# Kernel optimization log

Measured on AMD Instinct MI355X. Metric: run time of the kernel, lower is better.

The kernel has to match this reference:

```python
import jax, jax.numpy as jnp
import numpy as np

N_GRAPHS = 64
NEG_SLOPE = 0.01  # default LeakyReLU slope
BN_EPS = 1e-5


def setup_inputs() -> dict:
    key = jax.random.key(0)
    ks = jax.random.split(key, 16)
    N, E, F_IN, H, H2, OUT, L = 50000, 800000, 64, 128, 64, 8, 3
    return {
        "x": jax.random.normal(ks[0], (N, F_IN), jnp.float32),
        "edge_index": jax.random.randint(ks[1], (2, E), 0, N, jnp.int32),
        "batch": jnp.sort(jax.random.randint(ks[2], (N,), 0, N_GRAPHS, jnp.int32)),
        "W_emb": jax.random.normal(ks[3], (F_IN, H), jnp.float32) * 0.05,
        "b_emb": jnp.zeros((H,), jnp.float32),
        "convW": jax.random.normal(ks[4], (L, H, H), jnp.float32) * 0.05,
        "convB": jnp.zeros((L, H), jnp.float32),
        "bn_gamma": jax.random.uniform(ks[5], (L, H), jnp.float32) + 0.5,
        "bn_beta": jax.random.normal(ks[6], (L, H), jnp.float32) * 0.1,
        "bn_mean": jax.random.normal(ks[7], (L, H), jnp.float32) * 0.1,
        "bn_var": jax.random.uniform(ks[8], (L, H), jnp.float32) + 0.5,
        "W1": jax.random.normal(ks[9], (H, H2), jnp.float32) * 0.05,
        "b1": jnp.zeros((H2,), jnp.float32),
        "W2": jax.random.normal(ks[10], (H2, OUT), jnp.float32) * 0.05,
        "b2": jnp.zeros((OUT,), jnp.float32),
    }


def reference(x, edge_index, batch, W_emb, b_emb, convW, convB,
              bn_gamma, bn_beta, bn_mean, bn_var, W1, b1, W2, b2):
    N = x.shape[0]
    # GCN normalization with self-loops (computed once; identical per layer)
    loop = jnp.arange(N, dtype=edge_index.dtype)
    s = jnp.concatenate([edge_index[0], loop])  # [E+N]
    d = jnp.concatenate([edge_index[1], loop])
    deg = jax.ops.segment_sum(jnp.ones(d.shape, x.dtype), d, num_segments=N)
    dinv = jax.lax.rsqrt(deg)  # deg >= 1 thanks to self-loops
    norm = dinv[s] * dinv[d]  # [E+N]

    h = x @ W_emb + b_emb  # node embedding, [N, H]
    L = convW.shape[0]
    for i in range(L):
        m = h @ convW[i]  # linear transform, [N, H]
        # gather-weight-scatter: sum_{(s->d)} norm * m[s]
        agg = jax.ops.segment_sum(m[s] * norm[:, None], d, num_segments=N) + convB[i]
        # BatchNorm (eval mode, running stats)
        hbn = (agg - bn_mean[i]) * jax.lax.rsqrt(bn_var[i] + BN_EPS) * bn_gamma[i] + bn_beta[i]
        h = jnp.where(hbn > 0, hbn, NEG_SLOPE * hbn)  # LeakyReLU
        # dropout is identity in eval mode

    g = jax.ops.segment_sum(h, batch, num_segments=N_GRAPHS)  # global_add_pool, [G, H]
    z = g @ W1 + b1
    z = jnp.where(z > 0, z, NEG_SLOPE * z)
    return z @ W2 + b2  # [G, OUT]
```

## Files before the change

kernel.cpp:

```cpp
#include <hip/hip_runtime.h>

#define NEG 0.01f
#define HF 128
#define BK 64
#define PB 512
#define SEG 40

typedef __attribute__((ext_vector_type(8))) short bf8;
typedef __attribute__((ext_vector_type(4))) float f4;
typedef __attribute__((ext_vector_type(2))) float f2;

__device__ __forceinline__ unsigned short f2bf(float v) {
    unsigned u = __float_as_uint(v);
    u = (u + 0x7fff + ((u >> 16) & 1)) >> 16;
    return (unsigned short)u;
}

__global__ __launch_bounds__(256) void k_mega1(
        const int* __restrict__ src, const int* __restrict__ dst, int E,
        int* __restrict__ cellcnt, int2* __restrict__ binbuf,
        const float* __restrict__ x, const float* __restrict__ W_emb,
        const float* __restrict__ b_emb, short* __restrict__ hbuf, int N,
        const float* __restrict__ convW, short* __restrict__ wt_c, int L,
        int NBIN, int EB) {
    __shared__ short wt[128 * 88];
    __shared__ int lcur[256];
    const int bid = blockIdx.x;
    const int tid = threadIdx.x;

    if (bid < PB) {
        lcur[tid] = 0;
        __syncthreads();
        const int per = (E + PB - 1) / PB;
        const int e0 = bid * per;
        const int e1 = (e0 + per < E) ? e0 + per : E;
        for (int e = e0 + tid; e < e1; e += 256) {
            const int d = dst[e];
            const int b = d >> 8;
            const int p = atomicAdd(&lcur[b], 1);
            if (p < SEG)
                binbuf[((size_t)b * PB + bid) * SEG + p] = make_int2(src[e], d);
        }
        __syncthreads();
        if (tid < NBIN) {
            int c = lcur[tid];
            cellcnt[(size_t)tid * PB + bid] = c < SEG ? c : SEG;
        }
        return;
    }
    if (bid < PB + EB) {
        for (int i = tid; i < 128 * 64; i += 256) {
            const int n = i >> 6, k = i & 63;
            wt[n * 88 + k] = (short)f2bf(W_emb[(size_t)k * HF + n]);
        }
        __syncthreads();
        const int wid = tid >> 6, lane = tid & 63;
        const int lr = lane & 15, lk = lane >> 4;
        const int m0 = (bid - PB) * 64 + wid * 16;
        if (m0 >= N) return;
        const int arow_i = m0 + lr < N ? m0 + lr : N - 1;
        bf8 a[2];
        const float* arow = x + (size_t)arow_i * 64 + lk * 8;
#pragma unroll
        for (int kk = 0; kk < 2; ++kk) {
            const float4 p = *reinterpret_cast<const float4*>(arow + kk * 32);
            const float4 q = *reinterpret_cast<const float4*>(arow + kk * 32 + 4);
            bf8 t;
            t[0] = (short)f2bf(p.x); t[1] = (short)f2bf(p.y);
            t[2] = (short)f2bf(p.z); t[3] = (short)f2bf(p.w);
            t[4] = (short)f2bf(q.x); t[5] = (short)f2bf(q.y);
            t[6] = (short)f2bf(q.z); t[7] = (short)f2bf(q.w);
            a[kk] = t;
        }
#pragma unroll
        for (int n = 0; n < 8; ++n) {
            f4 acc = {0.f, 0.f, 0.f, 0.f};
            const short* brow = wt + (n * 16 + lr) * 88 + lk * 8;
#pragma unroll
            for (int kk = 0; kk < 2; ++kk) {
                const bf8 b = *reinterpret_cast<const bf8*>(brow + kk * 32);
                acc = __builtin_amdgcn_mfma_f32_16x16x32_bf16(a[kk], b, acc, 0, 0, 0);
            }
            const int col = n * 16 + lr;
            const float bs = b_emb[col];
#pragma unroll
            for (int r = 0; r < 4; ++r)
                hbuf[(size_t)(m0 + lk * 4 + r) * HF + col] = (short)f2bf(acc[r] + bs);
        }
        return;
    }
    const int i = (bid - PB - EB) * 256 + tid;
    const int per = HF * HF;
    if (i < L * per) {
        const int l = i / per, r = i % per;
        const int n = r / HF, k = r % HF;
        wt_c[i] = (short)f2bf(convW[(size_t)l * per + (size_t)k * HF + n]);
    }
}

__global__ __launch_bounds__(256) void k_binfill(
        const int* __restrict__ cellcnt, const int2* __restrict__ binbuf,
        int* __restrict__ bkt, int* __restrict__ cnt,
        float* __restrict__ gbuf, int NBIN) {
    const int bid = blockIdx.x;
    const int tid = threadIdx.x;
    if (bid >= NBIN) {
        for (int i = tid; i < 64 * HF; i += 256) gbuf[i] = 0.0f;
        return;
    }
    __shared__ int lcnt[256];
    lcnt[tid] = 0;
    __syncthreads();
    for (int sg = tid; sg < PB; sg += 256) {
        const int c = cellcnt[(size_t)bid * PB + sg];
        const int2* segp = binbuf + ((size_t)bid * PB + sg) * SEG;
        for (int i = 0; i < c; ++i) {
            const int2 ed = segp[i];
            const int p = atomicAdd(&lcnt[ed.y & 255], 1);
            if (p < BK) bkt[(size_t)ed.y * BK + p] = ed.x;
        }
    }
    __syncthreads();
    cnt[(bid << 8) + tid] = lcnt[tid];
}

__global__ __launch_bounds__(256) void k_gemm_conv(
        const short* __restrict__ A,
        const short* __restrict__ Bt,
        const int* __restrict__ cnt,
        short* __restrict__ C,
        int N) {
    const int tid = threadIdx.x;
    const int wid = tid >> 6, lane = tid & 63;
    const int lr = lane & 15, lk = lane >> 4;
    const int m0 = blockIdx.x * 128 + wid * 32;
    if (m0 >= N) return;
    bf8 aA[4], aB[4];
    const short* arowA = A + (size_t)(m0 + lr) * HF + lk * 8;
    const short* arowB = arowA + 16 * HF;
#pragma unroll
    for (int kk = 0; kk < 4; ++kk) {
        aA[kk] = *reinterpret_cast<const bf8*>(arowA + kk * 32);
        aB[kk] = *reinterpret_cast<const bf8*>(arowB + kk * 32);
    }
    float dvA[4], dvB[4];
#pragma unroll
    for (int r = 0; r < 4; ++r) {
        int rowA = m0 + lk * 4 + r;       if (rowA >= N) rowA = N - 1;
        int rowB = m0 + 16 + lk * 4 + r;  if (rowB >= N) rowB = N - 1;
        dvA[r] = rsqrtf((float)cnt[rowA] + 1.0f);
        dvB[r] = rsqrtf((float)cnt[rowB] + 1.0f);
    }
#pragma unroll
    for (int n = 0; n < 8; ++n) {
        f4 accA = {0.f, 0.f, 0.f, 0.f};
        f4 accB = {0.f, 0.f, 0.f, 0.f};
        const short* brow = Bt + (size_t)(n * 16 + lr) * HF + lk * 8;
#pragma unroll
        for (int kk = 0; kk < 4; ++kk) {
            const bf8 b = *reinterpret_cast<const bf8*>(brow + kk * 32);
            accA = __builtin_amdgcn_mfma_f32_16x16x32_bf16(aA[kk], b, accA, 0, 0, 0);
            accB = __builtin_amdgcn_mfma_f32_16x16x32_bf16(aB[kk], b, accB, 0, 0, 0);
        }
        const int col = n * 16 + lr;
#pragma unroll
        for (int r = 0; r < 4; ++r) {
            C[(size_t)(m0 + lk * 4 + r) * HF + col]      = (short)f2bf(accA[r] * dvA[r]);
            C[(size_t)(m0 + 16 + lk * 4 + r) * HF + col] = (short)f2bf(accB[r] * dvB[r]);
        }
    }
}

__global__ __launch_bounds__(256) void k_gather(
        const int* __restrict__ bkt, const int* __restrict__ cnt,
        const short* __restrict__ ms,
        const float* __restrict__ convB,
        const float* __restrict__ bn_g, const float* __restrict__ bn_b,
        const float* __restrict__ bn_m, const float* __restrict__ bn_v,
        short* __restrict__ h, int N) {
    const int wid  = (blockIdx.x * 256 + threadIdx.x) >> 6;
    const int lane = threadIdx.x & 63;
    const int sub  = lane >> 4;
    const int lf   = lane & 15;
    if (wid >= N) return;
    const size_t b0 = (size_t)wid * BK;
    const int myslot = bkt[b0 + lane];
    int deg = cnt[wid];
    if (deg > BK) deg = BK;

    f2 acc[4];
#pragma unroll
    for (int j = 0; j < 4; ++j) acc[j] = (f2){0.f, 0.f};
    union U { bf8 v; unsigned u[4]; };

    U self;
    self.v = *reinterpret_cast<const bf8*>(ms + (size_t)wid * HF + lf * 8);

    const int iters = (deg + 3) >> 2;
    int slot = sub;
    bool v0 = slot < deg;
    U r0;
    { const int s = v0 ? __shfl(myslot, slot) : wid;
      r0.v = *reinterpret_cast<const bf8*>(ms + (size_t)s * HF + lf * 8); }
    bool v1 = slot + 4 < deg;
    U r1;
    { const int s = v1 ? __shfl(myslot, slot + 4) : wid;
      r1.v = *reinterpret_cast<const bf8*>(ms + (size_t)s * HF + lf * 8); }
    for (int t = 0; t < iters; ++t) {
        const int sl2 = slot + 8;
        const bool v2 = sl2 < deg;
        const int s2 = v2 ? __shfl(myslot, sl2) : wid;
        U r2;
        r2.v = *reinterpret_cast<const bf8*>(ms + (size_t)s2 * HF + lf * 8);
        if (v0) {
#pragma unroll
            for (int j = 0; j < 4; ++j) {
                f2 val;
                val.x = __uint_as_float(r0.u[j] << 16);
                val.y = __uint_as_float(r0.u[j] & 0xffff0000u);
                acc[j] += val;
            }
        }
        r0 = r1; v0 = v1; r1 = r2; v1 = v2; slot += 4;
    }
    if (sub == 0) {
#pragma unroll
        for (int j = 0; j < 4; ++j) {
            f2 val;
            val.x = __uint_as_float(self.u[j] << 16);
            val.y = __uint_as_float(self.u[j] & 0xffff0000u);
            acc[j] += val;
        }
    }
#pragma unroll
    for (int j = 0; j < 4; ++j) {
        acc[j].x += __shfl_xor(acc[j].x, 16);
        acc[j].y += __shfl_xor(acc[j].y, 16);
        acc[j].x += __shfl_xor(acc[j].x, 32);
        acc[j].y += __shfl_xor(acc[j].y, 32);
    }
    if (sub == 0) {
        const float dv = rsqrtf((float)deg + 1.0f);
        const int f0 = lf * 8;
        unsigned ou[4];
#pragma unroll
        for (int j = 0; j < 4; ++j) {
            const int fx = f0 + 2 * j, fy = fx + 1;
            const float sx = rsqrtf(bn_v[fx] + 1e-5f) * bn_g[fx];
            const float sy = rsqrtf(bn_v[fy] + 1e-5f) * bn_g[fy];
            float vx = (dv * acc[j].x + convB[fx] - bn_m[fx]) * sx + bn_b[fx];
            float vy = (dv * acc[j].y + convB[fy] - bn_m[fy]) * sy + bn_b[fy];
            vx = vx > 0.0f ? vx : NEG * vx;
            vy = vy > 0.0f ? vy : NEG * vy;
            ou[j] = (unsigned)f2bf(vx) | ((unsigned)f2bf(vy) << 16);
        }
        *reinterpret_cast<uint4*>(h + (size_t)wid * HF + f0) =
            *reinterpret_cast<uint4*>(ou);
    }
}

__global__ __launch_bounds__(256) void k_pool(
        const short* __restrict__ h, const int* __restrict__ batch,
        float* __restrict__ g, int N, int per) {
    const int gwid = (blockIdx.x * 256 + threadIdx.x) >> 6;
    const int lane = threadIdx.x & 63;
    const int n0 = gwid * per;
    if (n0 >= N) return;
    const int n1 = (n0 + per < N) ? n0 + per : N;
    const int fp = lane * 2;
    float ax = 0.f, ay = 0.f;
    int cur = batch[n0];
    for (int n = n0; n < n1; ++n) {
        const int b = batch[n];
        if (b != cur) {
            atomicAdd(&g[cur * HF + fp], ax);
            atomicAdd(&g[cur * HF + fp + 1], ay);
            ax = 0.f; ay = 0.f; cur = b;
        }
        const unsigned u = *reinterpret_cast<const unsigned*>(h + (size_t)n * HF + fp);
        ax += __uint_as_float(u << 16);
        ay += __uint_as_float(u & 0xffff0000u);
    }
    atomicAdd(&g[cur * HF + fp], ax);
    atomicAdd(&g[cur * HF + fp + 1], ay);
}

__global__ __launch_bounds__(128) void k_mlp(
        const float* __restrict__ g, const float* __restrict__ W1,
        const float* __restrict__ b1, const float* __restrict__ W2,
        const float* __restrict__ b2, float* __restrict__ out) {
    __shared__ float gr[128];
    __shared__ float z[64];
    const int gid = blockIdx.x, t = threadIdx.x;
    gr[t] = g[gid * HF + t];
    __syncthreads();
    if (t < 64) {
        float acc = b1[t];
#pragma unroll 8
        for (int k = 0; k < 128; ++k) acc += gr[k] * W1[k * 64 + t];
        z[t] = acc > 0.0f ? acc : NEG * acc;
    }
    __syncthreads();
    if (t < 8) {
        float acc = b2[t];
#pragma unroll 8
        for (int j = 0; j < 64; ++j) acc += z[j] * W2[j * 8 + t];
        out[gid * 8 + t] = acc;
    }
}

extern "C" void kernel_launch(void* const* d_in, const int* in_sizes, int n_in,
                              void* d_out, int out_size, void* d_ws, size_t ws_size,
                              hipStream_t stream) {
    const float* x       = (const float*)d_in[0];
    const int*   eidx    = (const int*)  d_in[1];
    const int*   batch   = (const int*)  d_in[2];
    const float* W_emb   = (const float*)d_in[3];
    const float* b_emb   = (const float*)d_in[4];
    const float* convW   = (const float*)d_in[5];
    const float* convB   = (const float*)d_in[6];
    const float* bn_g    = (const float*)d_in[7];
    const float* bn_b    = (const float*)d_in[8];
    const float* bn_m    = (const float*)d_in[9];
    const float* bn_v    = (const float*)d_in[10];
    const float* W1      = (const float*)d_in[11];
    const float* b1      = (const float*)d_in[12];
    const float* W2      = (const float*)d_in[13];
    const float* b2      = (const float*)d_in[14];

    const int F_IN = 64;
    const int N = in_sizes[0] / F_IN;
    const int E = in_sizes[1] / 2;
    const int L = in_sizes[5] / (HF * HF);
    const int G = 64;

    const int* esrc = eidx;
    const int* edst = eidx + E;

    const int NBIN  = (N + 255) >> 8;
    const int Npad2 = NBIN << 8;
    const int Npad  = ((N + 127) / 128) * 128;

    int* bkt      = (int*)d_ws;
    int* cnt      = bkt + (size_t)Npad2 * BK;
    int* cellcnt  = cnt + Npad2;
    int2* binbuf  = (int2*)(cellcnt + (size_t)NBIN * PB);
    short* hbuf   = (short*)(binbuf + (size_t)NBIN * PB * SEG);
    short* ms     = hbuf + (size_t)Npad * HF;
    short* wt_c   = ms + (size_t)Npad * HF;
    float* gbuf   = (float*)(wt_c + (size_t)L * HF * HF);

    const int EB = (N + 63) / 64;
    const int WB = (L * HF * HF + 255) / 256;
    k_mega1<<<PB + EB + WB, 256, 0, stream>>>(
        esrc, edst, E, cellcnt, binbuf, x, W_emb, b_emb, hbuf, N,
        convW, wt_c, L, NBIN, EB);

    k_binfill<<<NBIN + 1, 256, 0, stream>>>(cellcnt, binbuf, bkt, cnt, gbuf, NBIN);

    for (int i = 0; i < L; ++i) {
        k_gemm_conv<<<(N + 127) / 128, 256, 0, stream>>>(
            hbuf, wt_c + (size_t)i * HF * HF, cnt, ms, N);
        k_gather<<<(N * 64 + 255) / 256, 256, 0, stream>>>(
            bkt, cnt, ms, convB + i * HF,
            bn_g + i * HF, bn_b + i * HF, bn_m + i * HF, bn_v + i * HF, hbuf, N);
    }

    const int nwaves = 256 * 4;
    const int per = (N + nwaves - 1) / nwaves;
    k_pool<<<256, 256, 0, stream>>>(hbuf, batch, gbuf, N, per);
    k_mlp<<<G, 128, 0, stream>>>(gbuf, W1, b1, W2, b2, (float*)d_out);
}
```

Before: 238.4 us.

## Pad neighbor buckets with zero-row offsets and precompute BN scale/shift

Neighbor buckets now hold byte offsets (index<<8) and are padded to a multiple of 8 with an offset pointing at a zeroed row placed after ms. This lets the gather loop run branch-free, issuing two independent loads per iteration without shuffle-index arithmetic or validity checks. BatchNorm scale and shift, with the conv bias folded in, are precomputed once per layer inside the setup mega-kernel, so the gather epilogue needs two float4 loads and an FMA instead of five scalar loads and an rsqrt. The padding adds some wasted loads of the zero row for low-degree nodes, and the byte-offset encoding limits node count to what fits in a 32-bit offset.

Measured after the change: 212.4 us. -10.9%, faster.

```diff
diff --git a/kernel.cpp b/kernel.cpp
--- a/kernel.cpp
+++ b/kernel.cpp
@@ -22,7 +22,11 @@
         const float* __restrict__ x, const float* __restrict__ W_emb,
         const float* __restrict__ b_emb, short* __restrict__ hbuf, int N,
         const float* __restrict__ convW, short* __restrict__ wt_c, int L,
-        int NBIN, int EB) {
+        const float* __restrict__ convB,
+        const float* __restrict__ bn_g, const float* __restrict__ bn_b,
+        const float* __restrict__ bn_m, const float* __restrict__ bn_v,
+        float* __restrict__ scb, float* __restrict__ shb,
+        int NBIN, int EB, int WB) {
     __shared__ short wt[128 * 88];
     __shared__ int lcur[256];
     const int bid = blockIdx.x;
@@ -89,23 +93,34 @@
         }
         return;
     }
-    const int i = (bid - PB - EB) * 256 + tid;
-    const int per = HF * HF;
-    if (i < L * per) {
-        const int l = i / per, r = i % per;
-        const int n = r / HF, k = r % HF;
-        wt_c[i] = (short)f2bf(convW[(size_t)l * per + (size_t)k * HF + n]);
+    if (bid < PB + EB + WB) {
+        const int i = (bid - PB - EB) * 256 + tid;
+        const int per = HF * HF;
+        if (i < L * per) {
+            const int l = i / per, r = i % per;
+            const int n = r / HF, k = r % HF;
+            wt_c[i] = (short)f2bf(convW[(size_t)l * per + (size_t)k * HF + n]);
+        }
+        return;
+    }
+    const int i = (bid - PB - EB - WB) * 256 + tid;
+    if (i < L * HF) {
+        const float s = rsqrtf(bn_v[i] + 1e-5f) * bn_g[i];
+        scb[i] = s;
+        shb[i] = (convB[i] - bn_m[i]) * s + bn_b[i];
     }
 }
 
 __global__ __launch_bounds__(256) void k_binfill(
         const int* __restrict__ cellcnt, const int2* __restrict__ binbuf,
         int* __restrict__ bkt, int* __restrict__ cnt,
-        float* __restrict__ gbuf, int NBIN) {
+        float* __restrict__ gbuf, short* __restrict__ mzero,
+        int NBIN, int ZROFF) {
     const int bid = blockIdx.x;
     const int tid = threadIdx.x;
     if (bid >= NBIN) {
         for (int i = tid; i < 64 * HF; i += 256) gbuf[i] = 0.0f;
+        if (tid < 64) reinterpret_cast<int*>(mzero)[tid] = 0;
         return;
     }
     __shared__ int lcnt[256];
@@ -117,11 +132,16 @@
         for (int i = 0; i < c; ++i) {
             const int2 ed = segp[i];
             const int p = atomicAdd(&lcnt[ed.y & 255], 1);
-            if (p < BK) bkt[(size_t)ed.y * BK + p] = ed.x;
+            if (p < BK) bkt[(size_t)ed.y * BK + p] = ed.x << 8;
         }
     }
     __syncthreads();
-    cnt[(bid << 8) + tid] = lcnt[tid];
+    int c = lcnt[tid];
+    if (c > BK) c = BK;
+    const int pc = (c + 7) & ~7;
+    const int node = (bid << 8) + tid;
+    for (int p = c; p < pc; ++p) bkt[(size_t)node * BK + p] = ZROFF;
+    cnt[node] = c;
 }
 
 __global__ __launch_bounds__(256) void k_gemm_conv(
@@ -174,9 +194,7 @@
 __global__ __launch_bounds__(256) void k_gather(
         const int* __restrict__ bkt, const int* __restrict__ cnt,
         const short* __restrict__ ms,
-        const float* __restrict__ convB,
-        const float* __restrict__ bn_g, const float* __restrict__ bn_b,
-        const float* __restrict__ bn_m, const float* __restrict__ bn_v,
+        const float* __restrict__ sc, const float* __restrict__ sh,
         short* __restrict__ h, int N) {
     const int wid  = (blockIdx.x * 256 + threadIdx.x) >> 6;
     const int lane = threadIdx.x & 63;
@@ -184,9 +202,9 @@
     const int lf   = lane & 15;
     if (wid >= N) return;
     const size_t b0 = (size_t)wid * BK;
-    const int myslot = bkt[b0 + lane];
-    int deg = cnt[wid];
-    if (deg > BK) deg = BK;
+    const int myoff = bkt[b0 + lane];
+    const int deg = cnt[wid];
+    const int pdeg = (deg + 7) & ~7;
 
     f2 acc[4];
 #pragma unroll
@@ -196,32 +214,22 @@
     U self;
     self.v = *reinterpret_cast<const bf8*>(ms + (size_t)wid * HF + lf * 8);
 
-    const int iters = (deg + 3) >> 2;
-    int slot = sub;
-    bool v0 = slot < deg;
-    U r0;
-    { const int s = v0 ? __shfl(myslot, slot) : wid;
-      r0.v = *reinterpret_cast<const bf8*>(ms + (size_t)s * HF + lf * 8); }
-    bool v1 = slot + 4 < deg;
-    U r1;
-    { const int s = v1 ? __shfl(myslot, slot + 4) : wid;
-      r1.v = *reinterpret_cast<const bf8*>(ms + (size_t)s * HF + lf * 8); }
-    for (int t = 0; t < iters; ++t) {
-        const int sl2 = slot + 8;
-        const bool v2 = sl2 < deg;
-        const int s2 = v2 ? __shfl(myslot, sl2) : wid;
-        U r2;
-        r2.v = *reinterpret_cast<const bf8*>(ms + (size_t)s2 * HF + lf * 8);
-        if (v0) {
-#pragma unroll
-            for (int j = 0; j < 4; ++j) {
-                f2 val;
-                val.x = __uint_as_float(r0.u[j] << 16);
-                val.y = __uint_as_float(r0.u[j] & 0xffff0000u);
-                acc[j] += val;
-            }
-        }
-        r0 = r1; v0 = v1; r1 = r2; v1 = v2; slot += 4;
+    const char* msb = (const char*)ms + lf * 16;
+    for (int t = sub; t < pdeg; t += 8) {
+        const int o0 = __shfl(myoff, t);
+        const int o1 = __shfl(myoff, t + 4);
+        U a, b;
+        a.v = *reinterpret_cast<const bf8*>(msb + o0);
+        b.v = *reinterpret_cast<const bf8*>(msb + o1);
+#pragma unroll
+        for (int j = 0; j < 4; ++j) {
+            f2 va, vb;
+            va.x = __uint_as_float(a.u[j] << 16);
+            va.y = __uint_as_float(a.u[j] & 0xffff0000u);
+            vb.x = __uint_as_float(b.u[j] << 16);
+            vb.y = __uint_as_float(b.u[j] & 0xffff0000u);
+            acc[j] += va + vb;
+        }
     }
     if (sub == 0) {
 #pragma unroll
@@ -242,16 +250,19 @@
     if (sub == 0) {
         const float dv = rsqrtf((float)deg + 1.0f);
         const int f0 = lf * 8;
+        const float4 sca = *reinterpret_cast<const float4*>(sc + f0);
+        const float4 scb2 = *reinterpret_cast<const float4*>(sc + f0 + 4);
+        const float4 sha = *reinterpret_cast<const float4*>(sh + f0);
+        const float4 shb2 = *reinterpret_cast<const float4*>(sh + f0 + 4);
+        const float scv[8] = {sca.x, sca.y, sca.z, sca.w, scb2.x, scb2.y, scb2.z, scb2.w};
+        const float shv[8] = {sha.x, sha.y, sha.z, sha.w, shb2.x, shb2.y, shb2.z, shb2.w};
         unsigned ou[4];
 #pragma unroll
         for (int j = 0; j < 4; ++j) {
-            const int fx = f0 + 2 * j, fy = fx + 1;
-            const float sx = rsqrtf(bn_v[fx] + 1e-5f) * bn_g[fx];
-            const float sy = rsqrtf(bn_v[fy] + 1e-5f) * bn_g[fy];
-            float vx = (dv * acc[j].x + convB[fx] - bn_m[fx]) * sx + bn_b[fx];
-            float vy = (dv * acc[j].y + convB[fy] - bn_m[fy]) * sy + bn_b[fy];
-            vx = vx > 0.0f ? vx : NEG * vx;
-            vy = vy > 0.0f ? vy : NEG * vy;
+            float vx = fmaf(acc[j].x * dv, scv[2 * j],     shv[2 * j]);
+            float vy = fmaf(acc[j].y * dv, scv[2 * j + 1], shv[2 * j + 1]);
+            vx = fmaxf(vx, NEG * vx);
+            vy = fmaxf(vy, NEG * vy);
             ou[j] = (unsigned)f2bf(vx) | ((unsigned)f2bf(vy) << 16);
         }
         *reinterpret_cast<uint4*>(h + (size_t)wid * HF + f0) =
@@ -347,23 +358,29 @@
     int2* binbuf  = (int2*)(cellcnt + (size_t)NBIN * PB);
     short* hbuf   = (short*)(binbuf + (size_t)NBIN * PB * SEG);
     short* ms     = hbuf + (size_t)Npad * HF;
-    short* wt_c   = ms + (size_t)Npad * HF;
+    short* wt_c   = ms + (size_t)(Npad + 128) * HF;
     float* gbuf   = (float*)(wt_c + (size_t)L * HF * HF);
+    float* scb    = gbuf + G * HF;
+    float* shb    = scb + L * HF;
+
+    const int ZROFF = Npad * HF * 2;
 
     const int EB = (N + 63) / 64;
     const int WB = (L * HF * HF + 255) / 256;
-    k_mega1<<<PB + EB + WB, 256, 0, stream>>>(
+    const int SB = (L * HF + 255) / 256;
+    k_mega1<<<PB + EB + WB + SB, 256, 0, stream>>>(
         esrc, edst, E, cellcnt, binbuf, x, W_emb, b_emb, hbuf, N,
-        convW, wt_c, L, NBIN, EB);
-
-    k_binfill<<<NBIN + 1, 256, 0, stream>>>(cellcnt, binbuf, bkt, cnt, gbuf, NBIN);
+        convW, wt_c, L, convB, bn_g, bn_b, bn_m, bn_v, scb, shb,
+        NBIN, EB, WB);
+
+    k_binfill<<<NBIN + 1, 256, 0, stream>>>(
+        cellcnt, binbuf, bkt, cnt, gbuf, ms + (size_t)Npad * HF, NBIN, ZROFF);
 
     for (int i = 0; i < L; ++i) {
         k_gemm_conv<<<(N + 127) / 128, 256, 0, stream>>>(
             hbuf, wt_c + (size_t)i * HF * HF, cnt, ms, N);
         k_gather<<<(N * 64 + 255) / 256, 256, 0, stream>>>(
-            bkt, cnt, ms, convB + i * HF,
-            bn_g + i * HF, bn_b + i * HF, bn_m + i * HF, bn_v + i * HF, hbuf, N);
+            bkt, cnt, ms, scb + i * HF, shb + i * HF, hbuf, N);
     }
 
     const int nwaves = 256 * 4;
```
